# Performance work log

Measured on AMD Instinct MI355X. Metric: run time of the kernel, lower is better.

## Reference

```python
import jax, jax.numpy as jnp
import numpy as np

ALPHA = 0.2

def _ema_last_weights(T, alpha, dtype):
    # Closed form for the final EMA value after the sequential recurrence:
    # ema_T = (1-a)^(T-1) * x_0 + sum_{t=1}^{T-1} a*(1-a)^(T-1-t) * x_t
    t = jnp.arange(T)
    w = alpha * (1.0 - alpha) ** (T - 1 - t)
    w = w.at[0].set((1.0 - alpha) ** (T - 1))
    return w.astype(dtype)


def setup_inputs() -> dict:
    key = jax.random.key(0)
    k1, k2 = jax.random.split(key)
    B, T, F = 64, 2048, 256
    x = jax.random.normal(k1, (B, T, F), dtype=jnp.float32)
    W = jax.random.normal(k2, (F, F), dtype=jnp.float32) * (1.0 / np.sqrt(F))
    b = jnp.zeros((F,), dtype=jnp.float32)
    return {"x": x, "W": W, "b": b}


def reference(x, W, b):
    B, T, F = x.shape
    # final-step EMA over time (equivalent to the sequential python loop)
    w = _ema_last_weights(T, ALPHA, x.dtype)          # [T]
    last_ref = jnp.einsum('t,btf->bf', w, x)[:, None, :]  # [B,1,F]
    # base residual predictor: per-timestep linear
    res = jnp.einsum('btf,fg->btg', x, W) + b          # [B,T,F]
    return last_ref + res
```

## Files before the change

kernel.cpp:

```cpp
#include <hip/hip_runtime.h>
#include <hip/hip_bf16.h>

#define Bdim 64
#define Tdim 2048
#define Fdim 256
#define TAIL 256
#define NCH 8
#define CHT 32

#define BM 64
#define BK 64
#define ASTR 72
#define BSTR 72

typedef __bf16 bf16x8 __attribute__((ext_vector_type(8)));
typedef float f32x16 __attribute__((ext_vector_type(16)));
typedef unsigned short u16x8 __attribute__((ext_vector_type(8)));

__device__ __forceinline__ unsigned short bf16_rne(float f) {
  unsigned int u = __float_as_uint(f);
  u += 0x7FFFu + ((u >> 16) & 1u);
  return (unsigned short)(u >> 16);
}

__global__ void prep_wt(const float* __restrict__ W, unsigned short* __restrict__ Wt) {
  int i = blockIdx.x * 256 + threadIdx.x;
  int g = i >> 8, f = i & 255;
  Wt[i] = bf16_rne(W[f * Fdim + g]);
}

__global__ void ema_partial(const float* __restrict__ x, float* __restrict__ part) {
  int b = blockIdx.x, c = blockIdx.y, f = threadIdx.x;
  int t0 = Tdim - TAIL + c * CHT;
  float w = 0.2f * exp2f((float)(Tdim - 1 - t0) * -0.32192809488736235f);
  const float* xp = x + ((size_t)b * Tdim + t0) * Fdim + f;
  float s = 0.f;
#pragma unroll
  for (int j = 0; j < CHT; ++j) {
    s += w * xp[(size_t)j * Fdim];
    w *= 1.25f;
  }
  part[(c * Bdim + b) * Fdim + f] = s;
}

__global__ __launch_bounds__(256, 3)
void gemm_fused(const float* __restrict__ x, const unsigned short* __restrict__ Wt,
                const float* __restrict__ bias, const float* __restrict__ part,
                float* __restrict__ out) {
  __shared__ unsigned short Abuf[BM * ASTR];
  __shared__ unsigned short Bbuf[Fdim * BSTR];
  __shared__ float lref[Fdim];

  const int tid = threadIdx.x;
  const int blk = blockIdx.x;
  const int b = blk >> 5;
  const size_t row0 = (size_t)blk * BM;

  {
    float s = bias[tid];
#pragma unroll
    for (int c = 0; c < NCH; ++c) s += part[(c * Bdim + b) * Fdim + tid];
    lref[tid] = s;
  }

  const int wave = tid >> 6;
  const int lane = tid & 63;
  const int lm = lane & 31;
  const int half = lane >> 5;

  f32x16 acc[2][2] = {};

  const int g8 = (tid & 7) * 8;
  const int arow = tid >> 3;

  for (int kc = 0; kc < 4; ++kc) {
    const int k0 = kc * BK;
#pragma unroll
    for (int p = 0; p < 2; ++p) {
      int r = arow + p * 32;
      const float* src = &x[(row0 + r) * Fdim + k0 + g8];
      float4 v0 = *(const float4*)src;
      float4 v1 = *(const float4*)(src + 4);
      u16x8 w;
      w[0] = bf16_rne(v0.x); w[1] = bf16_rne(v0.y);
      w[2] = bf16_rne(v0.z); w[3] = bf16_rne(v0.w);
      w[4] = bf16_rne(v1.x); w[5] = bf16_rne(v1.y);
      w[6] = bf16_rne(v1.z); w[7] = bf16_rne(v1.w);
      *(u16x8*)&Abuf[r * ASTR + g8] = w;
    }
#pragma unroll
    for (int p = 0; p < 8; ++p) {
      int n = arow + p * 32;
      u16x8 wv = *(const u16x8*)&Wt[n * Fdim + k0 + g8];
      *(u16x8*)&Bbuf[n * BSTR + g8] = wv;
    }
    __syncthreads();

    const int ko = half * 8;
#pragma unroll
    for (int s = 0; s < 4; ++s) {
      int kk = s * 16 + ko;
      bf16x8 a0 = *(const bf16x8*)&Abuf[(lm) * ASTR + kk];
      bf16x8 a1 = *(const bf16x8*)&Abuf[(32 + lm) * ASTR + kk];
      bf16x8 b0 = *(const bf16x8*)&Bbuf[(wave * 64 + lm) * BSTR + kk];
      bf16x8 b1 = *(const bf16x8*)&Bbuf[(wave * 64 + 32 + lm) * BSTR + kk];
      acc[0][0] = __builtin_amdgcn_mfma_f32_32x32x16_bf16(a0, b0, acc[0][0], 0, 0, 0);
      acc[0][1] = __builtin_amdgcn_mfma_f32_32x32x16_bf16(a0, b1, acc[0][1], 0, 0, 0);
      acc[1][0] = __builtin_amdgcn_mfma_f32_32x32x16_bf16(a1, b0, acc[1][0], 0, 0, 0);
      acc[1][1] = __builtin_amdgcn_mfma_f32_32x32x16_bf16(a1, b1, acc[1][1], 0, 0, 0);
    }
    __syncthreads();
  }

  float* op = out + row0 * Fdim;
  const int rbase = 4 * half;
#pragma unroll
  for (int i = 0; i < 2; ++i) {
#pragma unroll
    for (int j = 0; j < 2; ++j) {
      int n = wave * 64 + j * 32 + lm;
      float lb = lref[n];
#pragma unroll
      for (int r = 0; r < 16; ++r) {
        int rowi = i * 32 + (r & 3) + 8 * (r >> 2) + rbase;
        op[(size_t)rowi * Fdim + n] = acc[i][j][r] + lb;
      }
    }
  }
}

extern "C" void kernel_launch(void* const* d_in, const int* in_sizes, int n_in,
                              void* d_out, int out_size, void* d_ws, size_t ws_size,
                              hipStream_t stream) {
  const float* x = (const float*)d_in[0];
  const float* W = (const float*)d_in[1];
  const float* bias = (const float*)d_in[2];
  float* out = (float*)d_out;

  unsigned short* Wt = (unsigned short*)d_ws;
  float* part = (float*)((char*)d_ws + Fdim * Fdim * sizeof(unsigned short));

  prep_wt<<<Fdim, 256, 0, stream>>>(W, Wt);
  ema_partial<<<dim3(Bdim, NCH), 256, 0, stream>>>(x, part);
  gemm_fused<<<(Bdim * Tdim) / BM, 256, 0, stream>>>(x, Wt, bias, part, out);
}
```

Measured before the change: 244.2 us.

## Read W operand directly from global, stage full-K A tile, merge prep kernels

The GEMM kernel no longer stages the 256x256 bf16 weight matrix into shared memory. Each wave reads its B fragments straight from global/L2. The A tile is converted once for the full K=256 into a single padded LDS buffer, which removes the per-K-chunk barriers. The two small prep kernels are merged into one launch, and the bias plus EMA reference is kept in registers instead of LDS. This cuts LDS use, which can raise occupancy, and saves one launch, at the cost of repeated global loads of W from every block.

```diff
diff --git a/kernel.cpp b/kernel.cpp
--- a/kernel.cpp
+++ b/kernel.cpp
@@ -9,9 +9,7 @@
 #define CHT 32
 
 #define BM 64
-#define BK 64
-#define ASTR 72
-#define BSTR 72
+#define ASTR 264
 
 typedef __bf16 bf16x8 __attribute__((ext_vector_type(8)));
 typedef float f32x16 __attribute__((ext_vector_type(16)));
@@ -23,14 +21,19 @@
   return (unsigned short)(u >> 16);
 }
 
-__global__ void prep_wt(const float* __restrict__ W, unsigned short* __restrict__ Wt) {
-  int i = blockIdx.x * 256 + threadIdx.x;
-  int g = i >> 8, f = i & 255;
-  Wt[i] = bf16_rne(W[f * Fdim + g]);
-}
-
-__global__ void ema_partial(const float* __restrict__ x, float* __restrict__ part) {
-  int b = blockIdx.x, c = blockIdx.y, f = threadIdx.x;
+__global__ void prep(const float* __restrict__ x, const float* __restrict__ W,
+                     unsigned short* __restrict__ Wt, float* __restrict__ part) {
+  if (blockIdx.x >= 512) {
+    int base = (blockIdx.x - 512) * 1024 + threadIdx.x * 4;
+#pragma unroll
+    for (int j = 0; j < 4; ++j) {
+      int i = base + j;
+      int g = i >> 8, f = i & 255;
+      Wt[i] = bf16_rne(W[f * Fdim + g]);
+    }
+    return;
+  }
+  int b = blockIdx.x & 63, c = blockIdx.x >> 6, f = threadIdx.x;
   int t0 = Tdim - TAIL + c * CHT;
   float w = 0.2f * exp2f((float)(Tdim - 1 - t0) * -0.32192809488736235f);
   const float* xp = x + ((size_t)b * Tdim + t0) * Fdim + f;
@@ -48,68 +51,58 @@
                 const float* __restrict__ bias, const float* __restrict__ part,
                 float* __restrict__ out) {
   __shared__ unsigned short Abuf[BM * ASTR];
-  __shared__ unsigned short Bbuf[Fdim * BSTR];
-  __shared__ float lref[Fdim];
 
   const int tid = threadIdx.x;
   const int blk = blockIdx.x;
   const int b = blk >> 5;
   const size_t row0 = (size_t)blk * BM;
 
-  {
-    float s = bias[tid];
-#pragma unroll
-    for (int c = 0; c < NCH; ++c) s += part[(c * Bdim + b) * Fdim + tid];
-    lref[tid] = s;
-  }
-
   const int wave = tid >> 6;
   const int lane = tid & 63;
   const int lm = lane & 31;
   const int half = lane >> 5;
+  const int n0 = wave * 64 + lm;
+  const int n1 = n0 + 32;
 
-  f32x16 acc[2][2] = {};
+  float lb0 = bias[n0], lb1 = bias[n1];
+#pragma unroll
+  for (int c = 0; c < NCH; ++c) {
+    lb0 += part[(c * Bdim + b) * Fdim + n0];
+    lb1 += part[(c * Bdim + b) * Fdim + n1];
+  }
 
-  const int g8 = (tid & 7) * 8;
-  const int arow = tid >> 3;
-
-  for (int kc = 0; kc < 4; ++kc) {
-    const int k0 = kc * BK;
+  {
+    const int r = tid >> 2;
+    const int c0 = (tid & 3) * 64;
+    const float4* src = (const float4*)&x[(row0 + r) * Fdim + c0];
 #pragma unroll
-    for (int p = 0; p < 2; ++p) {
-      int r = arow + p * 32;
-      const float* src = &x[(row0 + r) * Fdim + k0 + g8];
-      float4 v0 = *(const float4*)src;
-      float4 v1 = *(const float4*)(src + 4);
+    for (int i = 0; i < 8; ++i) {
+      float4 v0 = src[2 * i];
+      float4 v1 = src[2 * i + 1];
       u16x8 w;
       w[0] = bf16_rne(v0.x); w[1] = bf16_rne(v0.y);
       w[2] = bf16_rne(v0.z); w[3] = bf16_rne(v0.w);
       w[4] = bf16_rne(v1.x); w[5] = bf16_rne(v1.y);
       w[6] = bf16_rne(v1.z); w[7] = bf16_rne(v1.w);
-      *(u16x8*)&Abuf[r * ASTR + g8] = w;
+      *(u16x8*)&Abuf[r * ASTR + c0 + i * 8] = w;
     }
-#pragma unroll
-    for (int p = 0; p < 8; ++p) {
-      int n = arow + p * 32;
-      u16x8 wv = *(const u16x8*)&Wt[n * Fdim + k0 + g8];
-      *(u16x8*)&Bbuf[n * BSTR + g8] = wv;
-    }
-    __syncthreads();
+  }
+  __syncthreads();
 
-    const int ko = half * 8;
-#pragma unroll
-    for (int s = 0; s < 4; ++s) {
-      int kk = s * 16 + ko;
-      bf16x8 a0 = *(const bf16x8*)&Abuf[(lm) * ASTR + kk];
-      bf16x8 a1 = *(const bf16x8*)&Abuf[(32 + lm) * ASTR + kk];
-      bf16x8 b0 = *(const bf16x8*)&Bbuf[(wave * 64 + lm) * BSTR + kk];
-      bf16x8 b1 = *(const bf16x8*)&Bbuf[(wave * 64 + 32 + lm) * BSTR + kk];
-      acc[0][0] = __builtin_amdgcn_mfma_f32_32x32x16_bf16(a0, b0, acc[0][0], 0, 0, 0);
-      acc[0][1] = __builtin_amdgcn_mfma_f32_32x32x16_bf16(a0, b1, acc[0][1], 0, 0, 0);
-      acc[1][0] = __builtin_amdgcn_mfma_f32_32x32x16_bf16(a1, b0, acc[1][0], 0, 0, 0);
-      acc[1][1] = __builtin_amdgcn_mfma_f32_32x32x16_bf16(a1, b1, acc[1][1], 0, 0, 0);
-    }
-    __syncthreads();
+  f32x16 acc[2][2] = {};
+  const int ko = half * 8;
+
+#pragma unroll 4
+  for (int s = 0; s < 16; ++s) {
+    const int kk = s * 16 + ko;
+    bf16x8 a0 = *(const bf16x8*)&Abuf[lm * ASTR + kk];
+    bf16x8 a1 = *(const bf16x8*)&Abuf[(32 + lm) * ASTR + kk];
+    bf16x8 b0 = *(const bf16x8*)&Wt[(size_t)n0 * Fdim + kk];
+    bf16x8 b1 = *(const bf16x8*)&Wt[(size_t)n1 * Fdim + kk];
+    acc[0][0] = __builtin_amdgcn_mfma_f32_32x32x16_bf16(a0, b0, acc[0][0], 0, 0, 0);
+    acc[0][1] = __builtin_amdgcn_mfma_f32_32x32x16_bf16(a0, b1, acc[0][1], 0, 0, 0);
+    acc[1][0] = __builtin_amdgcn_mfma_f32_32x32x16_bf16(a1, b0, acc[1][0], 0, 0, 0);
+    acc[1][1] = __builtin_amdgcn_mfma_f32_32x32x16_bf16(a1, b1, acc[1][1], 0, 0, 0);
   }
 
   float* op = out + row0 * Fdim;
@@ -118,8 +111,8 @@
   for (int i = 0; i < 2; ++i) {
 #pragma unroll
     for (int j = 0; j < 2; ++j) {
-      int n = wave * 64 + j * 32 + lm;
-      float lb = lref[n];
+      const int n = (j == 0) ? n0 : n1;
+      const float lb = (j == 0) ? lb0 : lb1;
 #pragma unroll
       for (int r = 0; r < 16; ++r) {
         int rowi = i * 32 + (r & 3) + 8 * (r >> 2) + rbase;
@@ -140,7 +133,6 @@
   unsigned short* Wt = (unsigned short*)d_ws;
   float* part = (float*)((char*)d_ws + Fdim * Fdim * sizeof(unsigned short));
 
-  prep_wt<<<Fdim, 256, 0, stream>>>(W, Wt);
-  ema_partial<<<dim3(Bdim, NCH), 256, 0, stream>>>(x, part);
+  prep<<<576, 256, 0, stream>>>(x, W, Wt, part);
   gemm_fused<<<(Bdim * Tdim) / BM, 256, 0, stream>>>(x, Wt, bias, part, out);
 }
```

Measured after the change: 271.9 us. 11.3% more time.
